# Kernel optimization log

Hardware: AMD Instinct MI355X
Metric: run time of the kernel (lower is better)

The kernel has to match this reference:

```python
import jax, jax.numpy as jnp
import numpy as np

NUM_GROUPS = 32
EPS = 1e-6


def setup_inputs() -> dict:
    key = jax.random.key(0)
    ks = jax.random.split(key, 4)
    B, C, H, W = 16, 512, 32, 32
    x = jax.random.normal(ks[0], (B, C, H, W), dtype=jnp.float32)
    norm_w = jnp.ones((C,), dtype=jnp.float32)
    norm_b = jnp.zeros((C,), dtype=jnp.float32)
    qkv_w = jax.random.normal(ks[1], (3 * C, C), dtype=jnp.float32) * (1.0 / np.sqrt(C))
    qkv_b = jnp.zeros((3 * C,), dtype=jnp.float32)
    proj_w = jax.random.normal(ks[2], (C, C), dtype=jnp.float32) * (1.0 / np.sqrt(C))
    proj_b = jnp.zeros((C,), dtype=jnp.float32)
    return {"x": x, "norm_w": norm_w, "norm_b": norm_b, "qkv_w": qkv_w,
            "qkv_b": qkv_b, "proj_w": proj_w, "proj_b": proj_b}


def _group_norm(x, w, b):
    B, C, H, W = x.shape
    g = NUM_GROUPS
    xg = x.reshape(B, g, C // g, H * W)
    mu = xg.mean(axis=(2, 3), keepdims=True)
    var = xg.var(axis=(2, 3), keepdims=True)
    xn = (xg - mu) * jax.lax.rsqrt(var + EPS)
    xn = xn.reshape(B, C, H, W)
    return xn * w[None, :, None, None] + b[None, :, None, None]


def reference(x, norm_w, norm_b, qkv_w, qkv_b, proj_w, proj_b):
    B, C, H, W = x.shape
    h = _group_norm(x, norm_w, norm_b)
    # 1x1 conv == channel GEMM
    qkv = jnp.einsum('oc,bchw->bohw', qkv_w, h) + qkv_b[None, :, None, None]
    q, k, v = jnp.split(qkv, 3, axis=1)
    N = H * W
    q = q.reshape(B, C, N)  # (b, c, n)
    k = k.reshape(B, C, N)
    v = v.reshape(B, C, N)
    scale = jnp.asarray(C, x.dtype) ** -0.5
    attn = jnp.einsum('bci,bcj->bij', q, k) * scale  # (b, Nq, Nk)
    attn = jax.nn.softmax(attn, axis=2)
    o = jnp.einsum('bcj,bij->bci', v, attn).reshape(B, C, H, W)
    out = jnp.einsum('oc,bchw->bohw', proj_w, o) + proj_b[None, :, None, None]
    return x + out
```

## Files before the change

kernel.cpp:

```cpp
#include <hip/hip_runtime.h>

typedef unsigned short u16;
typedef __bf16 bf16x8 __attribute__((ext_vector_type(8)));
typedef float f32x4 __attribute__((ext_vector_type(4)));

#define AS1 __attribute__((address_space(1)))
#define AS3 __attribute__((address_space(3)))


__device__ __forceinline__ u16 f2bf(float f) {
  union { float f; unsigned u; } v; v.f = f;
  return (u16)((v.u + 0x7fffu + ((v.u >> 16) & 1u)) >> 16);
}

__device__ __forceinline__ f32x4 mfma16(bf16x8 a, bf16x8 b, f32x4 c) {
  return __builtin_amdgcn_mfma_f32_16x16x32_bf16(a, b, c, 0, 0, 0);
}

template<int ROUNDS>
__device__ __forceinline__ void stage_mat(const u16* __restrict__ src, int ld,
                                          u16* lds, int wave, int lane) {
#pragma unroll
  for (int rnd = 0; rnd < ROUNDS; rnd++) {
    int rbase = rnd * 64 + wave * 8;
    int row = rbase + (lane >> 3);
    int slot = (lane & 7) ^ (row & 7);
    __builtin_amdgcn_global_load_lds(
        (const AS1 void*)(src + (size_t)row * ld + slot * 8),
        (AS3 void*)(lds + rbase * 64), 16, 0, 0);
  }
}

template<int M_REP, int NT>
__device__ __forceinline__ void gemm_core(const u16* __restrict__ A, int lda,
                                          const u16* __restrict__ B, int ldb,
                                          u16* lds, f32x4 (&acc)[M_REP][4],
                                          int wave, int lane) {
  constexpr int BM = M_REP * 32;
  constexpr int AR = BM / 64;
  constexpr int ATILE = BM * 64;
  constexpr int VM = AR + 4;
  u16* sA0 = lds;
  u16* sA1 = lds + ATILE;
  u16* sB0 = lds + 2 * ATILE;
  u16* sB1 = lds + 2 * ATILE + 16384;
  int wm = wave >> 2, wn = wave & 3;
  int col = lane & 15, rq = lane >> 4;
#pragma unroll
  for (int m = 0; m < M_REP; m++)
#pragma unroll
    for (int n = 0; n < 4; n++) acc[m][n] = (f32x4){0.f, 0.f, 0.f, 0.f};

  stage_mat<AR>(A, lda, sA0, wave, lane);
  stage_mat<4>(B, ldb, sB0, wave, lane);
  stage_mat<AR>(A + 64, lda, sA1, wave, lane);
  stage_mat<4>(B + 64, ldb, sB1, wave, lane);

  for (int t = 0; t < NT; t++) {
    u16* cA = (t & 1) ? sA1 : sA0;
    u16* cB = (t & 1) ? sB1 : sB0;
    if (t < NT - 1) {
      asm volatile("s_waitcnt vmcnt(%0)" :: "i"(VM) : "memory");
    } else {
      asm volatile("s_waitcnt vmcnt(0)" ::: "memory");
    }
    __builtin_amdgcn_sched_barrier(0);
    __builtin_amdgcn_s_barrier();
    __builtin_amdgcn_sched_barrier(0);
    __builtin_amdgcn_s_setprio(1);
#pragma unroll
    for (int kk = 0; kk < 2; kk++) {
      bf16x8 bfr[4];
#pragma unroll
      for (int n = 0; n < 4; n++) {
        int row = wn * 64 + n * 16 + col;
        bfr[n] = *(const bf16x8*)(cB + row * 64 + ((kk * 4 + rq) ^ (row & 7)) * 8);
      }
#pragma unroll
      for (int m = 0; m < M_REP; m++) {
        int row = wm * (BM / 2) + m * 16 + col;
        bf16x8 af = *(const bf16x8*)(cA + row * 64 + ((kk * 4 + rq) ^ (row & 7)) * 8);
#pragma unroll
        for (int n = 0; n < 4; n++) acc[m][n] = mfma16(af, bfr[n], acc[m][n]);
      }
    }
    __builtin_amdgcn_s_setprio(0);
    __builtin_amdgcn_sched_barrier(0);
    __builtin_amdgcn_s_barrier();
    if (t + 2 < NT) {
      stage_mat<AR>(A + (size_t)(t + 2) * 64, lda, cA, wave, lane);
      stage_mat<4>(B + (size_t)(t + 2) * 64, ldb, cB, wave, lane);
    }
  }
}

__global__ __launch_bounds__(256) void gn_stats(const float* __restrict__ x,
                                                float* __restrict__ mean,
                                                float* __restrict__ rstd) {
  int bg = blockIdx.x;
  const float4* p = (const float4*)(x + (size_t)bg * 16384);
  float s = 0.f, ss = 0.f;
  for (int i = threadIdx.x; i < 4096; i += 256) {
    float4 v = p[i];
    s  += v.x + v.y + v.z + v.w;
    ss += v.x*v.x + v.y*v.y + v.z*v.z + v.w*v.w;
  }
  for (int d = 32; d; d >>= 1) { s += __shfl_down(s, d); ss += __shfl_down(ss, d); }
  __shared__ float ls[4], lss[4];
  int wave = threadIdx.x >> 6;
  if ((threadIdx.x & 63) == 0) { ls[wave] = s; lss[wave] = ss; }
  __syncthreads();
  if (threadIdx.x == 0) {
    s = ls[0] + ls[1] + ls[2] + ls[3];
    ss = lss[0] + lss[1] + lss[2] + lss[3];
    float m = s * (1.f / 16384.f);
    float var = ss * (1.f / 16384.f) - m * m;
    mean[bg] = m;
    rstd[bg] = rsqrtf(var + 1e-6f);
  }
}

__global__ __launch_bounds__(256) void cast_bf16(const float* __restrict__ src,
                                                 u16* __restrict__ dst, int n) {
  int i = (blockIdx.x * 256 + threadIdx.x) * 4;
  if (i < n) {
    float4 v = *(const float4*)(src + i);
    dst[i] = f2bf(v.x); dst[i+1] = f2bf(v.y); dst[i+2] = f2bf(v.z); dst[i+3] = f2bf(v.w);
  }
}

__global__ __launch_bounds__(256) void gn_apply(const float* __restrict__ x,
                                                const float* __restrict__ mean,
                                                const float* __restrict__ rstd,
                                                const float* __restrict__ gw,
                                                const float* __restrict__ gb,
                                                u16* __restrict__ h) {
  __shared__ u16 tile[64][72];
  int b = blockIdx.z, c0 = blockIdx.y * 64, n0 = blockIdx.x * 64;
  int t = threadIdx.x;
  int cc = t >> 2, ns = (t & 3) * 16;
  int c = c0 + cc, g = c >> 4;
  float m = mean[b * 32 + g], r = rstd[b * 32 + g];
  float w = gw[c] * r;
  float bb = gb[c] - m * w;
  const float* xr = x + (((size_t)(b * 512 + c)) << 10) + n0 + ns;
#pragma unroll
  for (int u = 0; u < 16; u += 4) {
    float4 v = *(const float4*)(xr + u);
    tile[cc][ns + u + 0] = f2bf(v.x * w + bb);
    tile[cc][ns + u + 1] = f2bf(v.y * w + bb);
    tile[cc][ns + u + 2] = f2bf(v.z * w + bb);
    tile[cc][ns + u + 3] = f2bf(v.w * w + bb);
  }
  __syncthreads();
  int nn = t >> 2, cs = (t & 3) * 16;
  u16* hr = h + (((size_t)(b * 1024 + n0 + nn)) << 9) + c0 + cs;
  u16 vals[16];
#pragma unroll
  for (int u = 0; u < 16; u++) vals[u] = tile[cs + u][nn];
  *(uint4*)hr = *(uint4*)vals;
  *(uint4*)(hr + 8) = *(uint4*)(vals + 8);
}

__global__ __launch_bounds__(512, 1) void gemm_qkv(const u16* __restrict__ A,
                                                   const u16* __restrict__ Bn,
                                                   const float* __restrict__ bias,
                                                   u16* __restrict__ q_nc,
                                                   u16* __restrict__ k_nc,
                                                   u16* __restrict__ v) {
  __shared__ u16 lds[49152];
  int bid = blockIdx.x;
  int xcd = bid & 7, r = bid >> 3;
  int mb = r % 12, nb = xcd * 8 + r / 12;
  int m0 = mb * 128, n0 = nb * 256;
  int t = threadIdx.x, wave = t >> 6, lane = t & 63;
  int wm = wave >> 2, wn = wave & 3;
  int col = lane & 15, rq = lane >> 4;
  f32x4 acc[4][4];
  gemm_core<4, 8>(A + (size_t)m0 * 512, 512, Bn + (size_t)n0 * 512, 512,
                  lds, acc, wave, lane);
  if (mb < 8) {
    u16* dst = (mb < 4) ? q_nc : k_nc;
#pragma unroll
    for (int i = 0; i < 4; i++)
#pragma unroll
      for (int j = 0; j < 4; j++) {
        int o = m0 + wm * 64 + i * 16 + rq * 4;
        int bn = n0 + wn * 64 + j * 16 + col;
        u16 tmp[4];
#pragma unroll
        for (int rr = 0; rr < 4; rr++) tmp[rr] = f2bf(acc[i][j][rr] + bias[o + rr]);
        *(uint2*)(dst + (size_t)bn * 512 + (o & 511)) = *(uint2*)tmp;
      }
  } else {
#pragma unroll
    for (int i = 0; i < 4; i++)
#pragma unroll
      for (int j = 0; j < 4; j++)
#pragma unroll
        for (int rr = 0; rr < 4; rr++) {
          int o = m0 + wm * 64 + i * 16 + rq * 4 + rr;
          int bn = n0 + wn * 64 + j * 16 + col;
          v[(size_t)(o & 511) * 16384 + bn] = f2bf(acc[i][j][rr] + bias[o]);
        }
  }
}

__global__ __launch_bounds__(512, 1) void gemm_s(const u16* __restrict__ q_nc,
                                                 const u16* __restrict__ k_nc,
                                                 u16* __restrict__ E) {
  __shared__ u16 lds[65536];
  int bid = blockIdx.x;
  int xcd = bid & 7, r = bid >> 3;
  int b = xcd * 2 + (r & 1);
  int tile = r >> 1;
  int m0 = (tile >> 2) * 256, n0 = (tile & 3) * 256;
  int t = threadIdx.x, wave = t >> 6, lane = t & 63;
  int wm = wave >> 2, wn = wave & 3;
  int col = lane & 15, rq = lane >> 4;
  f32x4 acc[8][4];
  const u16* A  = q_nc + ((size_t)(b * 1024 + m0)) * 512;
  const u16* Bn = k_nc + ((size_t)(b * 1024 + n0)) * 512;
  gemm_core<8, 8>(A, 512, Bn, 512, lds, acc, wave, lane);
  u16* Eb = E + ((size_t)b << 20);
  const float scale = 0.04419417382415922f;
#pragma unroll
  for (int i = 0; i < 8; i++)
#pragma unroll
    for (int j = 0; j < 4; j++) {
      int ii = m0 + wm * 128 + i * 16 + rq * 4;
      int jj = n0 + wn * 64 + j * 16 + col;
#pragma unroll
      for (int rr = 0; rr < 4; rr++)
        Eb[(size_t)(ii + rr) * 1024 + jj] = f2bf(__expf(acc[i][j][rr] * scale));
    }
}

__global__ __launch_bounds__(256) void row_inv(const u16* __restrict__ E,
                                               float* __restrict__ inv) {
  int row = blockIdx.x * 4 + (threadIdx.x >> 6);
  int lane = threadIdx.x & 63;
  const u16* er = E + (size_t)row * 1024 + lane * 16;
  uint4 a = *(const uint4*)er;
  uint4 c = *(const uint4*)(er + 8);
  float s = 0.f;
  unsigned ws[8] = {a.x, a.y, a.z, a.w, c.x, c.y, c.z, c.w};
#pragma unroll
  for (int u = 0; u < 8; u++) {
    union { unsigned u; float f; } lo, hi;
    lo.u = ws[u] << 16; hi.u = ws[u] & 0xffff0000u;
    s += lo.f + hi.f;
  }
#pragma unroll
  for (int d = 1; d < 64; d <<= 1) s += __shfl_xor(s, d);
  if (lane == 0) inv[row] = 1.0f / s;
}

__global__ __launch_bounds__(512, 1) void gemm_pv(const u16* __restrict__ E,
                                                  const u16* __restrict__ v,
                                                  const float* __restrict__ inv,
                                                  u16* __restrict__ o_nc) {
  __shared__ u16 lds[49152];
  int bid = blockIdx.x;
  int xcd = bid & 7, r = bid >> 3;
  int b = xcd * 2 + (r & 1);
  int tile = r >> 1;
  int m0 = (tile >> 1) * 128, n0 = (tile & 1) * 256;
  int t = threadIdx.x, wave = t >> 6, lane = t & 63;
  int wm = wave >> 2, wn = wave & 3;
  int col = lane & 15, rq = lane >> 4;
  f32x4 acc[4][4];
  const u16* A  = E + ((size_t)b << 20) + (size_t)m0 * 1024;
  const u16* Bn = v + (size_t)n0 * 16384 + ((size_t)b << 10);
  gemm_core<4, 16>(A, 1024, Bn, 16384, lds, acc, wave, lane);
#pragma unroll
  for (int i = 0; i < 4; i++)
#pragma unroll
    for (int j = 0; j < 4; j++)
#pragma unroll
      for (int rr = 0; rr < 4; rr++) {
        int ii = m0 + wm * 64 + i * 16 + rq * 4 + rr;
        int cc = n0 + wn * 64 + j * 16 + col;
        float sc = inv[(b << 10) + ii];
        o_nc[(((size_t)(b * 1024 + ii)) << 9) + cc] = f2bf(acc[i][j][rr] * sc);
      }
}

__global__ __launch_bounds__(512, 1) void gemm_proj(const u16* __restrict__ A,
                                                    const u16* __restrict__ Bn,
                                                    const float* __restrict__ bias,
                                                    const float* __restrict__ xres,
                                                    float* __restrict__ outp) {
  __shared__ u16 lds[49152];
  int bid = blockIdx.x;
  int xcd = bid & 7, r = bid >> 3;
  int mb = r % 4, nb = xcd * 8 + r / 4;
  int m0 = mb * 128, n0 = nb * 256;
  int t = threadIdx.x, wave = t >> 6, lane = t & 63;
  int wm = wave >> 2, wn = wave & 3;
  int col = lane & 15, rq = lane >> 4;
  f32x4 acc[4][4];
  gemm_core<4, 8>(A + (size_t)m0 * 512, 512, Bn + (size_t)n0 * 512, 512,
                  lds, acc, wave, lane);
#pragma unroll
  for (int i = 0; i < 4; i++)
#pragma unroll
    for (int j = 0; j < 4; j++)
#pragma unroll
      for (int rr = 0; rr < 4; rr++) {
        int co = m0 + wm * 64 + i * 16 + rq * 4 + rr;
        int bn = n0 + wn * 64 + j * 16 + col;
        int bb = bn >> 10, n = bn & 1023;
        size_t oi = (((size_t)(bb * 512 + co)) << 10) + n;
        outp[oi] = acc[i][j][rr] + bias[co] + xres[oi];
      }
}

extern "C" void kernel_launch(void* const* d_in, const int* in_sizes, int n_in,
                              void* d_out, int out_size, void* d_ws, size_t ws_size,
                              hipStream_t stream) {
  const float* x      = (const float*)d_in[0];
  const float* norm_w = (const float*)d_in[1];
  const float* norm_b = (const float*)d_in[2];
  const float* qkv_w  = (const float*)d_in[3];
  const float* qkv_b  = (const float*)d_in[4];
  const float* proj_w = (const float*)d_in[5];
  const float* proj_b = (const float*)d_in[6];
  float* out = (float*)d_out;

  char* ws = (char*)d_ws;
  size_t off = 0;
  auto alloc = [&](size_t bytes) {
    void* p = ws + off;
    off += (bytes + 255) & ~(size_t)255;
    return p;
  };
  float* mean = (float*)alloc(512 * 4);
  float* rstd = (float*)alloc(512 * 4);
  float* inv  = (float*)alloc(16384 * 4);
  u16* wq   = (u16*)alloc((size_t)1536 * 512 * 2);
  u16* wp   = (u16*)alloc((size_t)512 * 512 * 2);
  u16* h    = (u16*)alloc((size_t)16384 * 512 * 2);
  u16* q_nc = (u16*)alloc((size_t)16384 * 512 * 2);
  u16* k_nc = (u16*)alloc((size_t)16384 * 512 * 2);
  u16* v    = (u16*)alloc((size_t)512 * 16384 * 2);
  u16* E    = (u16*)alloc((size_t)16 * 1024 * 1024 * 2);
  u16* o_nc = h;
  (void)in_sizes; (void)n_in; (void)out_size; (void)ws_size;

  gn_stats<<<512, 256, 0, stream>>>(x, mean, rstd);
  cast_bf16<<<(1536 * 512) / 1024, 256, 0, stream>>>(qkv_w, wq, 1536 * 512);
  cast_bf16<<<(512 * 512) / 1024, 256, 0, stream>>>(proj_w, wp, 512 * 512);
  gn_apply<<<dim3(16, 8, 16), 256, 0, stream>>>(x, mean, rstd, norm_w, norm_b, h);
  gemm_qkv<<<768, 512, 0, stream>>>(wq, h, qkv_b, q_nc, k_nc, v);
  gemm_s<<<256, 512, 0, stream>>>(q_nc, k_nc, E);
  row_inv<<<4096, 256, 0, stream>>>(E, inv);
  gemm_pv<<<256, 512, 0, stream>>>(E, v, inv, o_nc);
  gemm_proj<<<256, 512, 0, stream>>>(wp, o_nc, proj_b, x, out);
}
```

Baseline: 140.4 us.

## Shrink GEMM tiles to 128x128x32 with 256-thread blocks, fuse groupnorm and row sums

Every GEMM moves from large 512-thread tiles with 64-wide K steps to 128x128 tiles with 32-wide K steps, four waves and higher occupancy (launch bounds 256,4, smaller LDS), and a new swizzle and staging helper. GroupNorm stats and apply are merged into one kernel that buffers each group in LDS, so x is read once. The S GEMM epilogue now writes per-row partial exp sums, replacing a separate pass that re-read E with a tiny reduction kernel. Smaller tiles lower per-block data reuse and double the number of K iterations, but in exchange there are more blocks in flight.

```diff
diff --git a/kernel.cpp b/kernel.cpp
--- a/kernel.cpp
+++ b/kernel.cpp
@@ -17,106 +17,110 @@
   return __builtin_amdgcn_mfma_f32_16x16x32_bf16(a, b, c, 0, 0, 0);
 }
 
-template<int ROUNDS>
-__device__ __forceinline__ void stage_mat(const u16* __restrict__ src, int ld,
-                                          u16* lds, int wave, int lane) {
-#pragma unroll
-  for (int rnd = 0; rnd < ROUNDS; rnd++) {
-    int rbase = rnd * 64 + wave * 8;
-    int row = rbase + (lane >> 3);
-    int slot = (lane & 7) ^ (row & 7);
+__device__ __forceinline__ void stage_tile(const u16* __restrict__ src, size_t ld,
+                                           u16* lds, int wv, int lane) {
+#pragma unroll
+  for (int h2 = 0; h2 < 2; h2++) {
+    int rbase = wv * 32 + h2 * 16;
+    int row = rbase + (lane >> 2);
+    int segd = (lane & 3) ^ ((row >> 1) & 3);
     __builtin_amdgcn_global_load_lds(
-        (const AS1 void*)(src + (size_t)row * ld + slot * 8),
-        (AS3 void*)(lds + rbase * 64), 16, 0, 0);
-  }
-}
-
-template<int M_REP, int NT>
+        (const AS1 void*)(src + (size_t)row * ld + segd * 8),
+        (AS3 void*)(lds + rbase * 32), 16, 0, 0);
+  }
+}
+
+__device__ __forceinline__ bf16x8 ldsfrag(const u16* lds, int row, int rowq) {
+  int q = rowq ^ ((row >> 1) & 3);
+  return *(const bf16x8*)(lds + row * 32 + q * 8);
+}
+
+template<int NT>
 __device__ __forceinline__ void gemm_core(const u16* __restrict__ A, int lda,
                                           const u16* __restrict__ B, int ldb,
-                                          u16* lds, f32x4 (&acc)[M_REP][4],
+                                          u16* lds, f32x4 (&acc)[4][4],
                                           int wave, int lane) {
-  constexpr int BM = M_REP * 32;
-  constexpr int AR = BM / 64;
-  constexpr int ATILE = BM * 64;
-  constexpr int VM = AR + 4;
-  u16* sA0 = lds;
-  u16* sA1 = lds + ATILE;
-  u16* sB0 = lds + 2 * ATILE;
-  u16* sB1 = lds + 2 * ATILE + 16384;
-  int wm = wave >> 2, wn = wave & 3;
-  int col = lane & 15, rq = lane >> 4;
-#pragma unroll
-  for (int m = 0; m < M_REP; m++)
+  u16* sA0 = lds;        u16* sA1 = lds + 4096;
+  u16* sB0 = lds + 8192; u16* sB1 = lds + 12288;
+  int wm = wave >> 1, wn = wave & 1;
+  int col = lane & 15, rq = lane >> 4;
+#pragma unroll
+  for (int m = 0; m < 4; m++)
 #pragma unroll
     for (int n = 0; n < 4; n++) acc[m][n] = (f32x4){0.f, 0.f, 0.f, 0.f};
 
-  stage_mat<AR>(A, lda, sA0, wave, lane);
-  stage_mat<4>(B, ldb, sB0, wave, lane);
-  stage_mat<AR>(A + 64, lda, sA1, wave, lane);
-  stage_mat<4>(B + 64, ldb, sB1, wave, lane);
+  stage_tile(A, lda, sA0, wave, lane);
+  stage_tile(B, ldb, sB0, wave, lane);
+  stage_tile(A + 32, lda, sA1, wave, lane);
+  stage_tile(B + 32, ldb, sB1, wave, lane);
 
   for (int t = 0; t < NT; t++) {
     u16* cA = (t & 1) ? sA1 : sA0;
     u16* cB = (t & 1) ? sB1 : sB0;
     if (t < NT - 1) {
-      asm volatile("s_waitcnt vmcnt(%0)" :: "i"(VM) : "memory");
+      asm volatile("s_waitcnt vmcnt(4)" ::: "memory");
     } else {
       asm volatile("s_waitcnt vmcnt(0)" ::: "memory");
     }
     __builtin_amdgcn_sched_barrier(0);
     __builtin_amdgcn_s_barrier();
     __builtin_amdgcn_sched_barrier(0);
-    __builtin_amdgcn_s_setprio(1);
-#pragma unroll
-    for (int kk = 0; kk < 2; kk++) {
-      bf16x8 bfr[4];
-#pragma unroll
-      for (int n = 0; n < 4; n++) {
-        int row = wn * 64 + n * 16 + col;
-        bfr[n] = *(const bf16x8*)(cB + row * 64 + ((kk * 4 + rq) ^ (row & 7)) * 8);
-      }
-#pragma unroll
-      for (int m = 0; m < M_REP; m++) {
-        int row = wm * (BM / 2) + m * 16 + col;
-        bf16x8 af = *(const bf16x8*)(cA + row * 64 + ((kk * 4 + rq) ^ (row & 7)) * 8);
-#pragma unroll
-        for (int n = 0; n < 4; n++) acc[m][n] = mfma16(af, bfr[n], acc[m][n]);
-      }
-    }
-    __builtin_amdgcn_s_setprio(0);
+    bf16x8 af[4], bfr[4];
+#pragma unroll
+    for (int n = 0; n < 4; n++) bfr[n] = ldsfrag(cB, wn * 64 + n * 16 + col, rq);
+#pragma unroll
+    for (int m = 0; m < 4; m++) af[m] = ldsfrag(cA, wm * 64 + m * 16 + col, rq);
+#pragma unroll
+    for (int m = 0; m < 4; m++)
+#pragma unroll
+      for (int n = 0; n < 4; n++) acc[m][n] = mfma16(af[m], bfr[n], acc[m][n]);
     __builtin_amdgcn_sched_barrier(0);
     __builtin_amdgcn_s_barrier();
     if (t + 2 < NT) {
-      stage_mat<AR>(A + (size_t)(t + 2) * 64, lda, cA, wave, lane);
-      stage_mat<4>(B + (size_t)(t + 2) * 64, ldb, cB, wave, lane);
+      stage_tile(A + (size_t)(t + 2) * 32, lda, cA, wave, lane);
+      stage_tile(B + (size_t)(t + 2) * 32, ldb, cB, wave, lane);
     }
   }
 }
 
-__global__ __launch_bounds__(256) void gn_stats(const float* __restrict__ x,
-                                                float* __restrict__ mean,
-                                                float* __restrict__ rstd) {
+__global__ __launch_bounds__(256) void gn_fused(const float* __restrict__ x,
+                                                const float* __restrict__ gw,
+                                                const float* __restrict__ gb,
+                                                u16* __restrict__ h) {
+  __shared__ float buf[16 * 1032];
+  __shared__ float ls[4], lss[4];
   int bg = blockIdx.x;
+  int b = bg >> 5, g = bg & 31;
   const float4* p = (const float4*)(x + (size_t)bg * 16384);
   float s = 0.f, ss = 0.f;
   for (int i = threadIdx.x; i < 4096; i += 256) {
     float4 v = p[i];
+    int c = i >> 8, n = (i & 255) * 4;
+    *(float4*)&buf[c * 1032 + n] = v;
     s  += v.x + v.y + v.z + v.w;
     ss += v.x*v.x + v.y*v.y + v.z*v.z + v.w*v.w;
   }
   for (int d = 32; d; d >>= 1) { s += __shfl_down(s, d); ss += __shfl_down(ss, d); }
-  __shared__ float ls[4], lss[4];
-  int wave = threadIdx.x >> 6;
-  if ((threadIdx.x & 63) == 0) { ls[wave] = s; lss[wave] = ss; }
+  int wv = threadIdx.x >> 6;
+  if ((threadIdx.x & 63) == 0) { ls[wv] = s; lss[wv] = ss; }
   __syncthreads();
-  if (threadIdx.x == 0) {
-    s = ls[0] + ls[1] + ls[2] + ls[3];
-    ss = lss[0] + lss[1] + lss[2] + lss[3];
-    float m = s * (1.f / 16384.f);
-    float var = ss * (1.f / 16384.f) - m * m;
-    mean[bg] = m;
-    rstd[bg] = rsqrtf(var + 1e-6f);
+  float m = (ls[0] + ls[1] + ls[2] + ls[3]) * (1.f / 16384.f);
+  float var = (lss[0] + lss[1] + lss[2] + lss[3]) * (1.f / 16384.f) - m * m;
+  float r = rsqrtf(var + 1e-6f);
+  int c0 = g * 16;
+  float w[16], bb[16];
+#pragma unroll
+  for (int c = 0; c < 16; c++) {
+    w[c] = gw[c0 + c] * r;
+    bb[c] = gb[c0 + c] - m * w[c];
+  }
+  for (int n = threadIdx.x; n < 1024; n += 256) {
+    u16 o[16];
+#pragma unroll
+    for (int c = 0; c < 16; c++) o[c] = f2bf(buf[c * 1032 + n] * w[c] + bb[c]);
+    u16* dst = h + (((size_t)((b << 10) | n)) << 9) + c0;
+    *(uint4*)dst = *(uint4*)o;
+    *(uint4*)(dst + 8) = *(uint4*)(o + 8);
   }
 }
 
@@ -129,56 +133,23 @@
   }
 }
 
-__global__ __launch_bounds__(256) void gn_apply(const float* __restrict__ x,
-                                                const float* __restrict__ mean,
-                                                const float* __restrict__ rstd,
-                                                const float* __restrict__ gw,
-                                                const float* __restrict__ gb,
-                                                u16* __restrict__ h) {
-  __shared__ u16 tile[64][72];
-  int b = blockIdx.z, c0 = blockIdx.y * 64, n0 = blockIdx.x * 64;
-  int t = threadIdx.x;
-  int cc = t >> 2, ns = (t & 3) * 16;
-  int c = c0 + cc, g = c >> 4;
-  float m = mean[b * 32 + g], r = rstd[b * 32 + g];
-  float w = gw[c] * r;
-  float bb = gb[c] - m * w;
-  const float* xr = x + (((size_t)(b * 512 + c)) << 10) + n0 + ns;
-#pragma unroll
-  for (int u = 0; u < 16; u += 4) {
-    float4 v = *(const float4*)(xr + u);
-    tile[cc][ns + u + 0] = f2bf(v.x * w + bb);
-    tile[cc][ns + u + 1] = f2bf(v.y * w + bb);
-    tile[cc][ns + u + 2] = f2bf(v.z * w + bb);
-    tile[cc][ns + u + 3] = f2bf(v.w * w + bb);
-  }
-  __syncthreads();
-  int nn = t >> 2, cs = (t & 3) * 16;
-  u16* hr = h + (((size_t)(b * 1024 + n0 + nn)) << 9) + c0 + cs;
-  u16 vals[16];
-#pragma unroll
-  for (int u = 0; u < 16; u++) vals[u] = tile[cs + u][nn];
-  *(uint4*)hr = *(uint4*)vals;
-  *(uint4*)(hr + 8) = *(uint4*)(vals + 8);
-}
-
-__global__ __launch_bounds__(512, 1) void gemm_qkv(const u16* __restrict__ A,
+__global__ __launch_bounds__(256, 4) void gemm_qkv(const u16* __restrict__ A,
                                                    const u16* __restrict__ Bn,
                                                    const float* __restrict__ bias,
                                                    u16* __restrict__ q_nc,
                                                    u16* __restrict__ k_nc,
                                                    u16* __restrict__ v) {
-  __shared__ u16 lds[49152];
+  __shared__ u16 lds[16384];
   int bid = blockIdx.x;
   int xcd = bid & 7, r = bid >> 3;
-  int mb = r % 12, nb = xcd * 8 + r / 12;
-  int m0 = mb * 128, n0 = nb * 256;
+  int mb = r % 12, nb = xcd * 16 + r / 12;
+  int m0 = mb * 128, n0 = nb * 128;
   int t = threadIdx.x, wave = t >> 6, lane = t & 63;
-  int wm = wave >> 2, wn = wave & 3;
+  int wm = wave >> 1, wn = wave & 1;
   int col = lane & 15, rq = lane >> 4;
   f32x4 acc[4][4];
-  gemm_core<4, 8>(A + (size_t)m0 * 512, 512, Bn + (size_t)n0 * 512, 512,
-                  lds, acc, wave, lane);
+  gemm_core<16>(A + (size_t)m0 * 512, 512, Bn + (size_t)n0 * 512, 512,
+                lds, acc, wave, lane);
   if (mb < 8) {
     u16* dst = (mb < 4) ? q_nc : k_nc;
 #pragma unroll
@@ -206,102 +177,102 @@
   }
 }
 
-__global__ __launch_bounds__(512, 1) void gemm_s(const u16* __restrict__ q_nc,
+__global__ __launch_bounds__(256, 4) void gemm_s(const u16* __restrict__ q_nc,
                                                  const u16* __restrict__ k_nc,
-                                                 u16* __restrict__ E) {
-  __shared__ u16 lds[65536];
+                                                 u16* __restrict__ E,
+                                                 float* __restrict__ part) {
+  __shared__ u16 lds[16384];
   int bid = blockIdx.x;
   int xcd = bid & 7, r = bid >> 3;
   int b = xcd * 2 + (r & 1);
   int tile = r >> 1;
-  int m0 = (tile >> 2) * 256, n0 = (tile & 3) * 256;
+  int m0 = (tile >> 3) * 128, n0 = (tile & 7) * 128;
   int t = threadIdx.x, wave = t >> 6, lane = t & 63;
-  int wm = wave >> 2, wn = wave & 3;
-  int col = lane & 15, rq = lane >> 4;
-  f32x4 acc[8][4];
-  const u16* A  = q_nc + ((size_t)(b * 1024 + m0)) * 512;
-  const u16* Bn = k_nc + ((size_t)(b * 1024 + n0)) * 512;
-  gemm_core<8, 8>(A, 512, Bn, 512, lds, acc, wave, lane);
+  int wm = wave >> 1, wn = wave & 1;
+  int col = lane & 15, rq = lane >> 4;
+  f32x4 acc[4][4];
+  gemm_core<16>(q_nc + ((size_t)(b * 1024 + m0)) * 512, 512,
+                k_nc + ((size_t)(b * 1024 + n0)) * 512, 512,
+                lds, acc, wave, lane);
   u16* Eb = E + ((size_t)b << 20);
+  float* pb = part + ((size_t)b << 14);
+  int idx = (n0 >> 6) + wn;
   const float scale = 0.04419417382415922f;
 #pragma unroll
-  for (int i = 0; i < 8; i++)
-#pragma unroll
-    for (int j = 0; j < 4; j++) {
-      int ii = m0 + wm * 128 + i * 16 + rq * 4;
-      int jj = n0 + wn * 64 + j * 16 + col;
-#pragma unroll
-      for (int rr = 0; rr < 4; rr++)
-        Eb[(size_t)(ii + rr) * 1024 + jj] = f2bf(__expf(acc[i][j][rr] * scale));
+  for (int i = 0; i < 4; i++)
+#pragma unroll
+    for (int rr = 0; rr < 4; rr++) {
+      float e[4], rs = 0.f;
+#pragma unroll
+      for (int j = 0; j < 4; j++) { e[j] = __expf(acc[i][j][rr] * scale); rs += e[j]; }
+      rs += __shfl_xor(rs, 1); rs += __shfl_xor(rs, 2);
+      rs += __shfl_xor(rs, 4); rs += __shfl_xor(rs, 8);
+      int row = m0 + wm * 64 + i * 16 + rq * 4 + rr;
+      if (col == 0) pb[row * 16 + idx] = rs;
+#pragma unroll
+      for (int j = 0; j < 4; j++) {
+        int jj = n0 + wn * 64 + j * 16 + col;
+        Eb[(size_t)row * 1024 + jj] = f2bf(e[j]);
+      }
     }
 }
 
-__global__ __launch_bounds__(256) void row_inv(const u16* __restrict__ E,
-                                               float* __restrict__ inv) {
-  int row = blockIdx.x * 4 + (threadIdx.x >> 6);
-  int lane = threadIdx.x & 63;
-  const u16* er = E + (size_t)row * 1024 + lane * 16;
-  uint4 a = *(const uint4*)er;
-  uint4 c = *(const uint4*)(er + 8);
-  float s = 0.f;
-  unsigned ws[8] = {a.x, a.y, a.z, a.w, c.x, c.y, c.z, c.w};
-#pragma unroll
-  for (int u = 0; u < 8; u++) {
-    union { unsigned u; float f; } lo, hi;
-    lo.u = ws[u] << 16; hi.u = ws[u] & 0xffff0000u;
-    s += lo.f + hi.f;
-  }
-#pragma unroll
-  for (int d = 1; d < 64; d <<= 1) s += __shfl_xor(s, d);
-  if (lane == 0) inv[row] = 1.0f / s;
-}
-
-__global__ __launch_bounds__(512, 1) void gemm_pv(const u16* __restrict__ E,
+__global__ __launch_bounds__(256) void row_inv2(const float* __restrict__ part,
+                                                float* __restrict__ inv) {
+  int row = blockIdx.x * 256 + threadIdx.x;
+  const float4* p = (const float4*)(part + (size_t)row * 16);
+  float4 a = p[0], b = p[1], c = p[2], d = p[3];
+  float s = a.x+a.y+a.z+a.w + b.x+b.y+b.z+b.w + c.x+c.y+c.z+c.w + d.x+d.y+d.z+d.w;
+  inv[row] = 1.f / s;
+}
+
+__global__ __launch_bounds__(256, 4) void gemm_pv(const u16* __restrict__ E,
                                                   const u16* __restrict__ v,
                                                   const float* __restrict__ inv,
                                                   u16* __restrict__ o_nc) {
-  __shared__ u16 lds[49152];
+  __shared__ u16 lds[16384];
   int bid = blockIdx.x;
   int xcd = bid & 7, r = bid >> 3;
   int b = xcd * 2 + (r & 1);
   int tile = r >> 1;
-  int m0 = (tile >> 1) * 128, n0 = (tile & 1) * 256;
+  int m0 = (tile >> 2) * 128, n0 = (tile & 3) * 128;
   int t = threadIdx.x, wave = t >> 6, lane = t & 63;
-  int wm = wave >> 2, wn = wave & 3;
+  int wm = wave >> 1, wn = wave & 1;
   int col = lane & 15, rq = lane >> 4;
   f32x4 acc[4][4];
-  const u16* A  = E + ((size_t)b << 20) + (size_t)m0 * 1024;
-  const u16* Bn = v + (size_t)n0 * 16384 + ((size_t)b << 10);
-  gemm_core<4, 16>(A, 1024, Bn, 16384, lds, acc, wave, lane);
+  gemm_core<32>(E + ((size_t)b << 20) + (size_t)m0 * 1024, 1024,
+                v + (size_t)n0 * 16384 + ((size_t)b << 10), 16384,
+                lds, acc, wave, lane);
 #pragma unroll
   for (int i = 0; i < 4; i++)
 #pragma unroll
-    for (int j = 0; j < 4; j++)
-#pragma unroll
-      for (int rr = 0; rr < 4; rr++) {
-        int ii = m0 + wm * 64 + i * 16 + rq * 4 + rr;
+    for (int rr = 0; rr < 4; rr++) {
+      int ii = m0 + wm * 64 + i * 16 + rq * 4 + rr;
+      float sc = inv[(b << 10) + ii];
+#pragma unroll
+      for (int j = 0; j < 4; j++) {
         int cc = n0 + wn * 64 + j * 16 + col;
-        float sc = inv[(b << 10) + ii];
         o_nc[(((size_t)(b * 1024 + ii)) << 9) + cc] = f2bf(acc[i][j][rr] * sc);
       }
-}
-
-__global__ __launch_bounds__(512, 1) void gemm_proj(const u16* __restrict__ A,
+    }
+}
+
+__global__ __launch_bounds__(256, 4) void gemm_proj(const u16* __restrict__ A,
                                                     const u16* __restrict__ Bn,
                                                     const float* __restrict__ bias,
                                                     const float* __restrict__ xres,
                                                     float* __restrict__ outp) {
-  __shared__ u16 lds[49152];
+  __shared__ u16 lds[16384];
   int bid = blockIdx.x;
   int xcd = bid & 7, r = bid >> 3;
-  int mb = r % 4, nb = xcd * 8 + r / 4;
-  int m0 = mb * 128, n0 = nb * 256;
+  int mb = r & 3, nb = xcd * 16 + (r >> 2);
+  int m0 = mb * 128, n0 = nb * 128;
   int t = threadIdx.x, wave = t >> 6, lane = t & 63;
-  int wm = wave >> 2, wn = wave & 3;
+  int wm = wave >> 1, wn = wave & 1;
   int col = lane & 15, rq = lane >> 4;
   f32x4 acc[4][4];
-  gemm_core<4, 8>(A + (size_t)m0 * 512, 512, Bn + (size_t)n0 * 512, 512,
-                  lds, acc, wave, lane);
+  gemm_core<16>(A + (size_t)m0 * 512, 512, Bn + (size_t)n0 * 512, 512,
+                lds, acc, wave, lane);
 #pragma unroll
   for (int i = 0; i < 4; i++)
 #pragma unroll
@@ -335,8 +306,7 @@
     off += (bytes + 255) & ~(size_t)255;
     return p;
   };
-  float* mean = (float*)alloc(512 * 4);
-  float* rstd = (float*)alloc(512 * 4);
+  float* part = (float*)alloc((size_t)16384 * 16 * 4);
   float* inv  = (float*)alloc(16384 * 4);
   u16* wq   = (u16*)alloc((size_t)1536 * 512 * 2);
   u16* wp   = (u16*)alloc((size_t)512 * 512 * 2);
@@ -348,13 +318,12 @@
   u16* o_nc = h;
   (void)in_sizes; (void)n_in; (void)out_size; (void)ws_size;
 
-  gn_stats<<<512, 256, 0, stream>>>(x, mean, rstd);
+  gn_fused<<<512, 256, 0, stream>>>(x, norm_w, norm_b, h);
   cast_bf16<<<(1536 * 512) / 1024, 256, 0, stream>>>(qkv_w, wq, 1536 * 512);
   cast_bf16<<<(512 * 512) / 1024, 256, 0, stream>>>(proj_w, wp, 512 * 512);
-  gn_apply<<<dim3(16, 8, 16), 256, 0, stream>>>(x, mean, rstd, norm_w, norm_b, h);
-  gemm_qkv<<<768, 512, 0, stream>>>(wq, h, qkv_b, q_nc, k_nc, v);
-  gemm_s<<<256, 512, 0, stream>>>(q_nc, k_nc, E);
-  row_inv<<<4096, 256, 0, stream>>>(E, inv);
-  gemm_pv<<<256, 512, 0, stream>>>(E, v, inv, o_nc);
-  gemm_proj<<<256, 512, 0, stream>>>(wp, o_nc, proj_b, x, out);
-}
+  gemm_qkv<<<1536, 256, 0, stream>>>(wq, h, qkv_b, q_nc, k_nc, v);
+  gemm_s<<<1024, 256, 0, stream>>>(q_nc, k_nc, E, part);
+  row_inv2<<<64, 256, 0, stream>>>(part, inv);
+  gemm_pv<<<512, 256, 0, stream>>>(E, v, inv, o_nc);
+  gemm_proj<<<512, 256, 0, stream>>>(wp, o_nc, proj_b, x, out);
+}
```

After: 141.0 us. Within noise of the previous version (+0.4%).
